# Kernel tuning notes

Hardware: AMD Instinct MI355X
Metric: run time of the kernel (lower is better)

Reference implementation:

```python
import math
import jax, jax.numpy as jnp
import numpy as np

SEQ, BATCH, D_MODEL, HEADS = 2048, 2, 1024, 16
D_K = D_MODEL // HEADS


def setup_inputs() -> dict:
    key = jax.random.key(0)
    ks = jax.random.split(key, 11)
    s = 1.0 / math.sqrt(D_MODEL)
    inp = {
        "q": jax.random.normal(ks[0], (SEQ, BATCH, D_MODEL), jnp.float32),
        "k": jax.random.normal(ks[1], (SEQ, BATCH, D_MODEL), jnp.float32),
        "v": jax.random.normal(ks[2], (SEQ, BATCH, D_MODEL), jnp.float32),
        "Wq": jax.random.normal(ks[3], (D_MODEL, D_MODEL), jnp.float32) * s,
        "bq": jnp.zeros((D_MODEL,), jnp.float32),
        "Wk": jax.random.normal(ks[4], (D_MODEL, D_MODEL), jnp.float32) * s,
        "bk": jnp.zeros((D_MODEL,), jnp.float32),
        "Wv": jax.random.normal(ks[5], (D_MODEL, D_MODEL), jnp.float32) * s,
        "bv": jnp.zeros((D_MODEL,), jnp.float32),
        "Wo": jax.random.normal(ks[6], (D_MODEL, D_MODEL), jnp.float32) * s,
        "bo": jnp.zeros((D_MODEL,), jnp.float32),
    }
    return inp


def _proj(x, W, b):
    # [S,B,D] @ [D, H*Dk] -> [S,B,H,Dk]
    y = jnp.einsum('sbd,de->sbe', x, W) + b
    return y.reshape(x.shape[0], x.shape[1], HEADS, D_K)


def reference(q, k, v, Wq, bq, Wk, bk, Wv, bv, Wo, bo):
    scale = 1.0 / math.sqrt(D_K)
    query = _proj(q, Wq, bq)            # [i,b,h,d]
    key_ = _proj(k, Wk, bk)             # [j,b,h,d]
    value = _proj(v, Wv, bv)            # [j,b,h,d]
    scores = jnp.einsum('ibhd,jbhd->ijbh', query, key_) * scale
    attn = jax.nn.softmax(scores, axis=1)  # softmax over key axis j (dim=1)
    x = jnp.einsum('ijbh,jbhd->ibhd', attn, value)
    x = x.reshape(SEQ, BATCH, D_MODEL)
    return jnp.einsum('sbd,de->sbe', x, Wo) + bo
```

## Files before the change

kernel.cpp:

```cpp
#include <hip/hip_runtime.h>
#include <hip/hip_bf16.h>


typedef __attribute__((ext_vector_type(8))) short bf16x8;
typedef __attribute__((ext_vector_type(4))) float f32x4;

constexpr int SEQ   = 2048;
constexpr int BATCH = 2;
constexpr int DM    = 1024;
constexpr int DK    = 64;
constexpr int MR    = SEQ * BATCH;
constexpr int SST   = BATCH * DM;
constexpr int HD    = SEQ * DK;

__device__ __forceinline__ unsigned pkbf(float a, float b) {
    __hip_bfloat162 h = __float22bfloat162_rn(float2{a, b});
    union { __hip_bfloat162 h2; unsigned u; } cv;
    cv.h2 = h;
    return cv.u;
}

__device__ __forceinline__ f32x4 mfma16(bf16x8 a, bf16x8 b, f32x4 c) {
    return __builtin_amdgcn_mfma_f32_16x16x32_bf16(a, b, c, 0, 0, 0);
}

__device__ __forceinline__ void gl16(const unsigned short* g, unsigned short* l) {
    __builtin_amdgcn_global_load_lds(
        (const __attribute__((address_space(1))) void*)g,
        (__attribute__((address_space(3))) void*)l, 16, 0, 0);
}

__global__ __launch_bounds__(256)
void wt_prep_all(const float* __restrict__ w0, const float* __restrict__ w1,
                 const float* __restrict__ w2, const float* __restrict__ w3,
                 unsigned short* __restrict__ o0, unsigned short* __restrict__ o1,
                 unsigned short* __restrict__ o2, unsigned short* __restrict__ o3)
{
    const int z = blockIdx.z;
    const float* W = (z == 0) ? w0 : (z == 1) ? w1 : (z == 2) ? w2 : w3;
    unsigned short* Wt = (z == 0) ? o0 : (z == 1) ? o1 : (z == 2) ? o2 : o3;

    const int t = threadIdx.x;
    const int e = blockIdx.x * 64 + (t & 63);
    const int dq = blockIdx.y * 256 + (t >> 6) * 64;
    unsigned short* orow = Wt + (size_t)e * DM + dq;
#pragma unroll
    for (int c = 0; c < 8; ++c) {
        float f[8];
#pragma unroll
        for (int j = 0; j < 8; ++j)
            f[j] = W[(size_t)(dq + c * 8 + j) * DM + e];
        uint4 u = { pkbf(f[0], f[1]), pkbf(f[2], f[3]),
                    pkbf(f[4], f[5]), pkbf(f[6], f[7]) };
        *(uint4*)(orow + c * 8) = u;
    }
}

__global__ __launch_bounds__(256)
void qkv_cast(const float* __restrict__ qa, const float* __restrict__ ka,
              const float* __restrict__ va,
              unsigned short* __restrict__ Qb, unsigned short* __restrict__ Kb,
              unsigned short* __restrict__ Vb)
{
    const int z = blockIdx.y;
    const float* src = (z == 0) ? qa : (z == 1) ? ka : va;
    unsigned short* dst = (z == 0) ? Qb : (z == 1) ? Kb : Vb;
    const size_t i = ((size_t)blockIdx.x * 256 + threadIdx.x) * 8;
    float4 f0 = *(const float4*)(src + i);
    float4 f1 = *(const float4*)(src + i + 4);
    uint4 u = { pkbf(f0.x, f0.y), pkbf(f0.z, f0.w),
                pkbf(f1.x, f1.y), pkbf(f1.z, f1.w) };
    *(uint4*)(dst + i) = u;
}

__global__ __launch_bounds__(256)
void gemm_qkv_b(const unsigned short* __restrict__ Qb,
                const unsigned short* __restrict__ Kb,
                const unsigned short* __restrict__ Vb,
                const unsigned short* __restrict__ wq,
                const unsigned short* __restrict__ wk,
                const unsigned short* __restrict__ wv,
                const float* __restrict__ bq, const float* __restrict__ bk,
                const float* __restrict__ bv,
                unsigned short* __restrict__ Qh, unsigned short* __restrict__ Kh,
                unsigned short* __restrict__ Vtp)
{
    constexpr int K = 1024;
    __shared__ unsigned short As[2][128 * 32];
    __shared__ unsigned short Bs[2][128 * 32];

    const int z = blockIdx.z;
    const unsigned short* Ab = (z == 0) ? Qb : (z == 1) ? Kb : Vb;
    const unsigned short* Bt = (z == 0) ? wq : (z == 1) ? wk : wv;
    const float* bias = (z == 0) ? bq : (z == 1) ? bk : bv;

    const int l = blockIdx.x + 8 * blockIdx.y;
    const int xcd = l & 7, jj0 = l >> 3;
    const int bm = xcd * 4 + (jj0 >> 3);
    const int bn = jj0 & 7;

    const int tid = threadIdx.x;
    const int wave = tid >> 6, lane = tid & 63;
    const int wr = wave >> 1, wc = wave & 1;
    const int lrow = lane & 15, g = lane >> 4;
    const int gr = lane & 15, gc = (lane >> 4) * 8;

    const unsigned short* aRow0 = Ab + (size_t)(bm * 128 + wave * 32 + gr) * K + gc;
    const unsigned short* aRow1 = aRow0 + (size_t)16 * K;
    const unsigned short* bRow0 = Bt + (size_t)(bn * 128 + wave * 32 + gr) * K + gc;
    const unsigned short* bRow1 = bRow0 + (size_t)16 * K;

    f32x4 acc[4][4] = {};

    auto stageA = [&](int k0) {
        gl16(aRow0 + k0, As[0] + (2 * wave) * 512);
        gl16(aRow1 + k0, As[0] + (2 * wave + 1) * 512);
        gl16(bRow0 + k0, Bs[0] + (2 * wave) * 512);
        gl16(bRow1 + k0, Bs[0] + (2 * wave + 1) * 512);
    };
    auto stageB = [&](int k0) {
        gl16(aRow0 + k0, As[1] + (2 * wave) * 512);
        gl16(aRow1 + k0, As[1] + (2 * wave + 1) * 512);
        gl16(bRow0 + k0, Bs[1] + (2 * wave) * 512);
        gl16(bRow1 + k0, Bs[1] + (2 * wave + 1) * 512);
    };
    auto compute = [&](const unsigned short* as, const unsigned short* bs) {
        bf16x8 af[4], bfr[4];
#pragma unroll
        for (int i = 0; i < 4; ++i)
            af[i] = *(const bf16x8*)&as[(wr * 4 + i) * 512 + lane * 8];
#pragma unroll
        for (int j = 0; j < 4; ++j)
            bfr[j] = *(const bf16x8*)&bs[(wc * 4 + j) * 512 + lane * 8];
        __builtin_amdgcn_s_setprio(1);
#pragma unroll
        for (int i = 0; i < 4; ++i)
#pragma unroll
            for (int j = 0; j < 4; ++j)
                acc[i][j] = mfma16(af[i], bfr[j], acc[i][j]);
        __builtin_amdgcn_s_setprio(0);
    };

    stageA(0);
    asm volatile("s_waitcnt vmcnt(0)" ::: "memory");
    __syncthreads();

#pragma unroll 1
    for (int k0 = 0; k0 < K; k0 += 64) {
        stageB(k0 + 32);
        compute(As[0], Bs[0]);
        __syncthreads();
        if (k0 + 64 < K) stageA(k0 + 64);
        compute(As[1], Bs[1]);
        __syncthreads();
    }

#pragma unroll
    for (int j = 0; j < 4; ++j) {
        const int col = bn * 128 + wc * 64 + j * 16 + lrow;
        const float bb = bias[col];
        const int h = col >> 6, d = col & 63;
#pragma unroll
        for (int i = 0; i < 4; ++i) {
            const int row0 = bm * 128 + wr * 64 + i * 16 + 4 * g;
#pragma unroll
            for (int r = 0; r < 4; ++r) {
                const float v = acc[i][j][r] + bb;
                const unsigned short bfv = (unsigned short)(pkbf(v, v) & 0xffffu);
                const int row = row0 + r;
                const int s = row >> 1, b = row & 1;
                if (z != 2) {
                    unsigned short* C = (z == 0) ? Qh : Kh;
                    C[(size_t)(b * 16 + h) * HD + s * 64 + d] = bfv;
                } else {
                    const int st = s >> 6, sl = s & 63;
                    const int kc = sl >> 5, r5 = sl & 31;
                    const int h2 = r5 >> 4, gg = (r5 >> 2) & 3, jv = r5 & 3;
                    const int sp = kc * 32 + gg * 8 + h2 * 4 + jv;
                    Vtp[(size_t)(b * 16 + h) * HD + (size_t)d * SEQ + st * 64 + sp] = bfv;
                }
            }
        }
    }
}

__global__ __launch_bounds__(256)
void attn_mfma(const unsigned short* __restrict__ Qh,
               const unsigned short* __restrict__ Kh,
               const unsigned short* __restrict__ Vtp,
               unsigned short* __restrict__ Xp)
{
    __shared__ unsigned short lds[16384];

    const int tid = threadIdx.x;
    const int fid = blockIdx.x;
    const int xcd = fid & 7, idx = fid >> 3;
    const int bh = xcd * 4 + (idx >> 4);
    const int qt = idx & 15;

    const int wave = tid >> 6, lane = tid & 63;
    const int lrow = lane & 15, g = lane >> 4;
    const int s7 = lrow & 7;
    const int q0w = qt * 128 + wave * 32;
    const float CE = 0.18033688011112042592f;

    const unsigned short* qb = Qh + (size_t)bh * HD;
    const unsigned short* kb = Kh + (size_t)bh * HD;
    const unsigned short* vb = Vtp + (size_t)bh * HD;

    unsigned short* K0 = lds;
    unsigned short* V0 = lds + 4096;
    unsigned short* K1 = lds + 8192;
    unsigned short* V1 = lds + 12288;

    const int r8 = lane >> 3, c8 = lane & 7;
    const unsigned short* ksrcA = kb + (size_t)(wave * 16 + r8) * 64 + (c8 ^ r8) * 8;
    const unsigned short* ksrcB = ksrcA + 8 * 64;
    const unsigned short* vsrcA = vb + (size_t)(wave * 16 + r8) * SEQ + (c8 ^ r8) * 8;
    const unsigned short* vsrcB = vsrcA + 8 * SEQ;

    auto stage = [&](unsigned short* kbuf, unsigned short* vbuf, int t) {
        const size_t ko = (size_t)t * 4096;
        const size_t vo = (size_t)t * 64;
        gl16(ksrcA + ko, kbuf + wave * 1024);
        gl16(ksrcB + ko, kbuf + wave * 1024 + 512);
        gl16(vsrcA + vo, vbuf + wave * 1024);
        gl16(vsrcB + vo, vbuf + wave * 1024 + 512);
    };

    bf16x8 bq[2][2];
#pragma unroll
    for (int qi = 0; qi < 2; ++qi)
#pragma unroll
        for (int dc = 0; dc < 2; ++dc)
            bq[qi][dc] = *(const bf16x8*)(qb + (size_t)(q0w + qi * 16 + lrow) * 64
                                             + dc * 32 + g * 8);

    f32x4 oacc[4][2] = {};
    float lsum0 = 0.f, lsum1 = 0.f;

    const int off0 = lrow * 64 + ((g ^ s7) * 8);
    const int off1 = lrow * 64 + (((4 + g) ^ s7) * 8);

    auto compute = [&](const unsigned short* kbuf, const unsigned short* vbuf) {
        bf16x8 ak[4][2];
#pragma unroll
        for (int kt = 0; kt < 4; ++kt) {
            ak[kt][0] = *(const bf16x8*)(kbuf + kt * 1024 + off0);
            ak[kt][1] = *(const bf16x8*)(kbuf + kt * 1024 + off1);
        }

        uint4 pbu[2][2];
#pragma unroll
        for (int qi = 0; qi < 2; ++qi) {
            float ll = 0.f;
#pragma unroll
            for (int kt = 0; kt < 4; ++kt) {
                f32x4 s = { 0.f, 0.f, 0.f, 0.f };
                s = mfma16(ak[kt][0], bq[qi][0], s);
                s = mfma16(ak[kt][1], bq[qi][1], s);
                const float p0 = __builtin_amdgcn_exp2f(s[0] * CE);
                const float p1 = __builtin_amdgcn_exp2f(s[1] * CE);
                const float p2 = __builtin_amdgcn_exp2f(s[2] * CE);
                const float p3 = __builtin_amdgcn_exp2f(s[3] * CE);
                ll += (p0 + p1) + (p2 + p3);
                const unsigned lo = pkbf(p0, p1);
                const unsigned hi = pkbf(p2, p3);
                if (kt & 1) { pbu[kt >> 1][qi].z = lo; pbu[kt >> 1][qi].w = hi; }
                else        { pbu[kt >> 1][qi].x = lo; pbu[kt >> 1][qi].y = hi; }
            }
            if (qi == 0) lsum0 += ll; else lsum1 += ll;
        }

        bf16x8 av[4][2];
#pragma unroll
        for (int dt = 0; dt < 4; ++dt) {
            av[dt][0] = *(const bf16x8*)(vbuf + dt * 1024 + off0);
            av[dt][1] = *(const bf16x8*)(vbuf + dt * 1024 + off1);
        }

        __builtin_amdgcn_s_setprio(1);
#pragma unroll
        for (int kc = 0; kc < 2; ++kc)
#pragma unroll
            for (int dt = 0; dt < 4; ++dt)
#pragma unroll
                for (int qi = 0; qi < 2; ++qi) {
                    union { uint4 u; bf16x8 v; } cv;
                    cv.u = pbu[kc][qi];
                    oacc[dt][qi] = mfma16(av[dt][kc], cv.v, oacc[dt][qi]);
                }
        __builtin_amdgcn_s_setprio(0);
    };

    stage(K0, V0, 0);
    asm volatile("s_waitcnt vmcnt(0)" ::: "memory");
    __syncthreads();

#pragma unroll 1
    for (int tt = 0; tt < 16; ++tt) {
        stage(K1, V1, 2 * tt + 1);
        compute(K0, V0);
        __syncthreads();
        if (tt < 15) stage(K0, V0, 2 * tt + 2);
        compute(K1, V1);
        __syncthreads();
    }

    float l0 = lsum0; l0 += __shfl_xor(l0, 16); l0 += __shfl_xor(l0, 32);
    float l1 = lsum1; l1 += __shfl_xor(l1, 16); l1 += __shfl_xor(l1, 32);
    const float inv0 = 1.0f / l0, inv1 = 1.0f / l1;

    unsigned short (*osh)[72] = (unsigned short (*)[72])(lds + wave * 32 * 72);
#pragma unroll
    for (int qi = 0; qi < 2; ++qi) {
        const float inv = qi ? inv1 : inv0;
#pragma unroll
        for (int dt = 0; dt < 4; ++dt) {
            const int d0 = dt * 16 + 4 * g;
            const unsigned u0 = pkbf(oacc[dt][qi][0] * inv, oacc[dt][qi][1] * inv);
            const unsigned u1 = pkbf(oacc[dt][qi][2] * inv, oacc[dt][qi][3] * inv);
            *(unsigned*)&osh[qi * 16 + lrow][d0] = u0;
            *(unsigned*)&osh[qi * 16 + lrow][d0 + 2] = u1;
        }
    }
    const int ql = lane >> 1;
    const int dh = (lane & 1) * 32;
    unsigned short* xrow = Xp + (size_t)(q0w + ql) * SST + bh * 64 + dh;
#pragma unroll
    for (int c = 0; c < 4; ++c) {
        uint4 vv = *(const uint4*)&osh[ql][dh + c * 8];
        *(uint4*)(xrow + c * 8) = vv;
    }
}

__global__ __launch_bounds__(256)
void gemm_out(const unsigned short* __restrict__ Xp,
              const unsigned short* __restrict__ WtO,
              const float* __restrict__ bias, float* __restrict__ out)
{
    constexpr int K = 1024, N = 1024;
    __shared__ unsigned short As[2][128 * 32];
    __shared__ unsigned short Bs[2][64 * 32];

    const int l = blockIdx.x + 16 * blockIdx.y;
    const int xcd = l & 7, jj0 = l >> 3;
    const int bm = xcd * 4 + (jj0 >> 4);
    const int bn = jj0 & 15;

    const int tid = threadIdx.x;
    const int wave = tid >> 6, lane = tid & 63;
    const int wr = wave >> 1, wc = wave & 1;
    const int lrow = lane & 15, g = lane >> 4;
    const int gr = lane & 15, gc = (lane >> 4) * 8;

    const unsigned short* aRow0 = Xp + (size_t)(bm * 128 + wave * 32 + gr) * K + gc;
    const unsigned short* aRow1 = aRow0 + (size_t)16 * K;
    const unsigned short* bRow0 = WtO + (size_t)(bn * 64 + wave * 16 + gr) * K + gc;

    f32x4 acc[4][2] = {};

    auto stageA = [&](int k0) {
        gl16(aRow0 + k0, As[0] + (2 * wave) * 512);
        gl16(aRow1 + k0, As[0] + (2 * wave + 1) * 512);
        gl16(bRow0 + k0, Bs[0] + wave * 512);
    };
    auto stageB = [&](int k0) {
        gl16(aRow0 + k0, As[1] + (2 * wave) * 512);
        gl16(aRow1 + k0, As[1] + (2 * wave + 1) * 512);
        gl16(bRow0 + k0, Bs[1] + wave * 512);
    };
    auto compute = [&](const unsigned short* as, const unsigned short* bs) {
        bf16x8 af[4], bfr[2];
#pragma unroll
        for (int i = 0; i < 4; ++i)
            af[i] = *(const bf16x8*)&as[(wr * 4 + i) * 512 + lane * 8];
#pragma unroll
        for (int j = 0; j < 2; ++j)
            bfr[j] = *(const bf16x8*)&bs[(wc * 2 + j) * 512 + lane * 8];
        __builtin_amdgcn_s_setprio(1);
#pragma unroll
        for (int i = 0; i < 4; ++i)
#pragma unroll
            for (int j = 0; j < 2; ++j)
                acc[i][j] = mfma16(af[i], bfr[j], acc[i][j]);
        __builtin_amdgcn_s_setprio(0);
    };

    stageA(0);
    asm volatile("s_waitcnt vmcnt(0)" ::: "memory");
    __syncthreads();

#pragma unroll 1
    for (int k0 = 0; k0 < K; k0 += 64) {
        stageB(k0 + 32);
        compute(As[0], Bs[0]);
        __syncthreads();
        if (k0 + 64 < K) stageA(k0 + 64);
        compute(As[1], Bs[1]);
        __syncthreads();
    }

#pragma unroll
    for (int j = 0; j < 2; ++j) {
        const int col = bn * 64 + wc * 32 + j * 16 + lrow;
        const float bb = bias[col];
#pragma unroll
        for (int i = 0; i < 4; ++i) {
            const int row0 = bm * 128 + wr * 64 + i * 16 + 4 * g;
#pragma unroll
            for (int r = 0; r < 4; ++r)
                out[(size_t)(row0 + r) * N + col] = acc[i][j][r] + bb;
        }
    }
}

extern "C" void kernel_launch(void* const* d_in, const int* in_sizes, int n_in,
                              void* d_out, int out_size, void* d_ws, size_t ws_size,
                              hipStream_t stream) {
    (void)in_sizes; (void)n_in; (void)out_size; (void)ws_size;

    const float* q  = (const float*)d_in[0];
    const float* k  = (const float*)d_in[1];
    const float* v  = (const float*)d_in[2];
    const float* Wq = (const float*)d_in[3];
    const float* bq = (const float*)d_in[4];
    const float* Wk = (const float*)d_in[5];
    const float* bk = (const float*)d_in[6];
    const float* Wv = (const float*)d_in[7];
    const float* bv = (const float*)d_in[8];
    const float* Wo = (const float*)d_in[9];
    const float* bo = (const float*)d_in[10];
    float* out = (float*)d_out;

    unsigned short* ws = (unsigned short*)d_ws;
    const size_t WSZ = (size_t)DM * DM;
    const size_t MSZ = (size_t)MR * DM;
    unsigned short* WtQ = ws;
    unsigned short* WtK = ws + WSZ;
    unsigned short* WtV = ws + 2 * WSZ;
    unsigned short* WtO = ws + 3 * WSZ;
    unsigned short* Qb  = ws + 4 * WSZ;
    unsigned short* Kb  = Qb + MSZ;
    unsigned short* Vb  = Kb + MSZ;
    unsigned short* Qh  = Vb + MSZ;
    unsigned short* Kh  = Qh + MSZ;
    unsigned short* Vtp = Kh + MSZ;
    unsigned short* Xp  = Vtp + MSZ;

    const dim3 blk(256);

    wt_prep_all<<<dim3(16, 4, 4), blk, 0, stream>>>(Wq, Wk, Wv, Wo, WtQ, WtK, WtV, WtO);

    qkv_cast<<<dim3(2048, 3), blk, 0, stream>>>(q, k, v, Qb, Kb, Vb);

    gemm_qkv_b<<<dim3(8, 32, 3), blk, 0, stream>>>(Qb, Kb, Vb, WtQ, WtK, WtV,
                                                   bq, bk, bv, Qh, Kh, Vtp);

    attn_mfma<<<dim3(512), blk, 0, stream>>>(Qh, Kh, Vtp, Xp);

    gemm_out<<<dim3(16, 32), blk, 0, stream>>>(Xp, WtO, bo, out);
}
```

Baseline: 154.3 us.

## Restructure projection GEMM main loops into a two-stage prefetch pipeline with partial waits

```diff
diff --git a/kernel.cpp b/kernel.cpp
--- a/kernel.cpp
+++ b/kernel.cpp
@@ -112,26 +112,28 @@
 
     f32x4 acc[4][4] = {};
 
-    auto stageA = [&](int k0) {
+    auto stage0 = [&](int k0) {
         gl16(aRow0 + k0, As[0] + (2 * wave) * 512);
         gl16(aRow1 + k0, As[0] + (2 * wave + 1) * 512);
         gl16(bRow0 + k0, Bs[0] + (2 * wave) * 512);
         gl16(bRow1 + k0, Bs[0] + (2 * wave + 1) * 512);
     };
-    auto stageB = [&](int k0) {
+    auto stage1 = [&](int k0) {
         gl16(aRow0 + k0, As[1] + (2 * wave) * 512);
         gl16(aRow1 + k0, As[1] + (2 * wave + 1) * 512);
         gl16(bRow0 + k0, Bs[1] + (2 * wave) * 512);
         gl16(bRow1 + k0, Bs[1] + (2 * wave + 1) * 512);
     };
-    auto compute = [&](const unsigned short* as, const unsigned short* bs) {
-        bf16x8 af[4], bfr[4];
+    auto loadFrag = [&](bf16x8 (&af)[4], bf16x8 (&bfr)[4],
+                        const unsigned short* as, const unsigned short* bs) {
 #pragma unroll
         for (int i = 0; i < 4; ++i)
             af[i] = *(const bf16x8*)&as[(wr * 4 + i) * 512 + lane * 8];
 #pragma unroll
         for (int j = 0; j < 4; ++j)
             bfr[j] = *(const bf16x8*)&bs[(wc * 4 + j) * 512 + lane * 8];
+    };
+    auto domfma = [&](bf16x8 (&af)[4], bf16x8 (&bfr)[4]) {
         __builtin_amdgcn_s_setprio(1);
 #pragma unroll
         for (int i = 0; i < 4; ++i)
@@ -141,18 +143,47 @@
         __builtin_amdgcn_s_setprio(0);
     };
 
-    stageA(0);
-    asm volatile("s_waitcnt vmcnt(0)" ::: "memory");
-    __syncthreads();
+    stage0(0);
+    stage1(32);
 
 #pragma unroll 1
-    for (int k0 = 0; k0 < K; k0 += 64) {
-        stageB(k0 + 32);
-        compute(As[0], Bs[0]);
-        __syncthreads();
-        if (k0 + 64 < K) stageA(k0 + 64);
-        compute(As[1], Bs[1]);
-        __syncthreads();
+    for (int k0 = 0; k0 < 960; k0 += 64) {
+        asm volatile("s_waitcnt vmcnt(4)" ::: "memory");
+        __builtin_amdgcn_s_barrier();
+        {
+            bf16x8 af[4], bfr[4];
+            loadFrag(af, bfr, As[0], Bs[0]);
+            asm volatile("s_waitcnt lgkmcnt(0)" ::: "memory");
+            __builtin_amdgcn_sched_barrier(0);
+            __builtin_amdgcn_s_barrier();
+            stage0(k0 + 64);
+            domfma(af, bfr);
+        }
+        asm volatile("s_waitcnt vmcnt(4)" ::: "memory");
+        __builtin_amdgcn_s_barrier();
+        {
+            bf16x8 af[4], bfr[4];
+            loadFrag(af, bfr, As[1], Bs[1]);
+            asm volatile("s_waitcnt lgkmcnt(0)" ::: "memory");
+            __builtin_amdgcn_sched_barrier(0);
+            __builtin_amdgcn_s_barrier();
+            stage1(k0 + 96);
+            domfma(af, bfr);
+        }
+    }
+    {
+        asm volatile("s_waitcnt vmcnt(4)" ::: "memory");
+        __builtin_amdgcn_s_barrier();
+        bf16x8 af[4], bfr[4];
+        loadFrag(af, bfr, As[0], Bs[0]);
+        domfma(af, bfr);
+    }
+    {
+        asm volatile("s_waitcnt vmcnt(0)" ::: "memory");
+        __builtin_amdgcn_s_barrier();
+        bf16x8 af[4], bfr[4];
+        loadFrag(af, bfr, As[1], Bs[1]);
+        domfma(af, bfr);
     }
 
 #pragma unroll
@@ -360,24 +391,26 @@
 
     f32x4 acc[4][2] = {};
 
-    auto stageA = [&](int k0) {
+    auto stage0 = [&](int k0) {
         gl16(aRow0 + k0, As[0] + (2 * wave) * 512);
         gl16(aRow1 + k0, As[0] + (2 * wave + 1) * 512);
         gl16(bRow0 + k0, Bs[0] + wave * 512);
     };
-    auto stageB = [&](int k0) {
+    auto stage1 = [&](int k0) {
         gl16(aRow0 + k0, As[1] + (2 * wave) * 512);
         gl16(aRow1 + k0, As[1] + (2 * wave + 1) * 512);
         gl16(bRow0 + k0, Bs[1] + wave * 512);
     };
-    auto compute = [&](const unsigned short* as, const unsigned short* bs) {
-        bf16x8 af[4], bfr[2];
+    auto loadFrag = [&](bf16x8 (&af)[4], bf16x8 (&bfr)[2],
+                        const unsigned short* as, const unsigned short* bs) {
 #pragma unroll
         for (int i = 0; i < 4; ++i)
             af[i] = *(const bf16x8*)&as[(wr * 4 + i) * 512 + lane * 8];
 #pragma unroll
         for (int j = 0; j < 2; ++j)
             bfr[j] = *(const bf16x8*)&bs[(wc * 2 + j) * 512 + lane * 8];
+    };
+    auto domfma = [&](bf16x8 (&af)[4], bf16x8 (&bfr)[2]) {
         __builtin_amdgcn_s_setprio(1);
 #pragma unroll
         for (int i = 0; i < 4; ++i)
@@ -387,18 +420,47 @@
         __builtin_amdgcn_s_setprio(0);
     };
 
-    stageA(0);
-    asm volatile("s_waitcnt vmcnt(0)" ::: "memory");
-    __syncthreads();
+    stage0(0);
+    stage1(32);
 
 #pragma unroll 1
-    for (int k0 = 0; k0 < K; k0 += 64) {
-        stageB(k0 + 32);
-        compute(As[0], Bs[0]);
-        __syncthreads();
-        if (k0 + 64 < K) stageA(k0 + 64);
-        compute(As[1], Bs[1]);
-        __syncthreads();
+    for (int k0 = 0; k0 < 960; k0 += 64) {
+        asm volatile("s_waitcnt vmcnt(3)" ::: "memory");
+        __builtin_amdgcn_s_barrier();
+        {
+            bf16x8 af[4], bfr[2];
+            loadFrag(af, bfr, As[0], Bs[0]);
+            asm volatile("s_waitcnt lgkmcnt(0)" ::: "memory");
+            __builtin_amdgcn_sched_barrier(0);
+            __builtin_amdgcn_s_barrier();
+            stage0(k0 + 64);
+            domfma(af, bfr);
+        }
+        asm volatile("s_waitcnt vmcnt(3)" ::: "memory");
+        __builtin_amdgcn_s_barrier();
+        {
+            bf16x8 af[4], bfr[2];
+            loadFrag(af, bfr, As[1], Bs[1]);
+            asm volatile("s_waitcnt lgkmcnt(0)" ::: "memory");
+            __builtin_amdgcn_sched_barrier(0);
+            __builtin_amdgcn_s_barrier();
+            stage1(k0 + 96);
+            domfma(af, bfr);
+        }
+    }
+    {
+        asm volatile("s_waitcnt vmcnt(3)" ::: "memory");
+        __builtin_amdgcn_s_barrier();
+        bf16x8 af[4], bfr[2];
+        loadFrag(af, bfr, As[0], Bs[0]);
+        domfma(af, bfr);
+    }
+    {
+        asm volatile("s_waitcnt vmcnt(0)" ::: "memory");
+        __builtin_amdgcn_s_barrier();
+        bf16x8 af[4], bfr[2];
+        loadFrag(af, bfr, As[1], Bs[1]);
+        domfma(af, bfr);
     }
 
 #pragma unroll
```

Result: no change. 153.5 us (-0.6%).
